# Kernel tuning notes

Measured on AMD Instinct MI355X. Metric: run time of the kernel, lower is better.

The kernel has to match this reference:

```python
import jax, jax.numpy as jnp
import numpy as np

B, T, I, H, O = 8192, 180, 7, 64, 16

def setup_inputs() -> dict:
    key = jax.random.key(0)
    ks = jax.random.split(key, 8)
    s_ih = 1.0 / np.sqrt(H)
    x = jax.random.normal(ks[0], (B, T, I), dtype=jnp.float32)
    # PyTorch nn.LSTM param layout: [4H, in] with gate order i, f, g, o
    W_ih = jax.random.uniform(ks[1], (4 * H, I), jnp.float32, -s_ih, s_ih)
    W_hh = jax.random.uniform(ks[2], (4 * H, H), jnp.float32, -s_ih, s_ih)
    b_ih = jax.random.uniform(ks[3], (4 * H,), jnp.float32, -s_ih, s_ih)
    b_hh = jax.random.uniform(ks[4], (4 * H,), jnp.float32, -s_ih, s_ih)
    W_fc = jax.random.uniform(ks[5], (O, H), jnp.float32, -s_ih, s_ih)
    b_fc = jax.random.uniform(ks[6], (O,), jnp.float32, -s_ih, s_ih)
    return {"x": x, "W_ih": W_ih, "W_hh": W_hh, "b_ih": b_ih,
            "b_hh": b_hh, "W_fc": W_fc, "b_fc": b_fc}

def reference(x, W_ih, W_hh, b_ih, b_hh, W_fc, b_fc):
    x = x.reshape(-1, T, I)
    b = b_ih + b_hh
    # precompute input projections for all timesteps: [T, B, 4H]
    xg = jnp.einsum('bti,gi->tbg', x, W_ih) + b

    def step(carry, xg_t):
        h, c = carry
        gates = xg_t + h @ W_hh.T  # [B, 4H]
        i_g, f_g, g_g, o_g = jnp.split(gates, 4, axis=-1)
        i_g = jax.nn.sigmoid(i_g)
        f_g = jax.nn.sigmoid(f_g)
        g_g = jnp.tanh(g_g)
        o_g = jax.nn.sigmoid(o_g)
        c = f_g * c + i_g * g_g
        h = o_g * jnp.tanh(c)
        return (h, c), None

    h0 = jnp.zeros((x.shape[0], H), dtype=x.dtype)
    c0 = jnp.zeros((x.shape[0], H), dtype=x.dtype)
    (h_last, _), _ = jax.lax.scan(step, (h0, c0), xg)
    return h_last @ W_fc.T + b_fc  # [B, O]
```

## Files before the change

### kernel.cpp

```cpp
#include <hip/hip_runtime.h>
#include <math.h>

#ifndef __has_builtin
#define __has_builtin(x) 0
#endif

#if __has_builtin(__builtin_amdgcn_rcpf)
#define FAST_RCP(x) __builtin_amdgcn_rcpf(x)
#else
#define FAST_RCP(x) (1.0f / (x))
#endif

#if __has_builtin(__builtin_amdgcn_exp2f)
#define FAST_EXP2(x) __builtin_amdgcn_exp2f(x)
#else
#define FAST_EXP2(x) exp2f(x)
#endif

typedef _Float16 half8 __attribute__((ext_vector_type(8)));
typedef _Float16 half2v __attribute__((ext_vector_type(2)));
typedef float f32x4 __attribute__((ext_vector_type(4)));
typedef float f32x2 __attribute__((ext_vector_type(2)));

constexpr int T_STEPS  = 180;
constexpr int I_DIM    = 7;
constexpr int HDIM     = 64;
constexpr int BT       = 16;
constexpr int BSTRIDE  = 104;

__global__ __launch_bounds__(512, 4) void lstm_mfma_kernel(
    const float* __restrict__ x,
    const float* __restrict__ W_ih,
    const float* __restrict__ W_hh,
    const float* __restrict__ b_ih,
    const float* __restrict__ b_hh,
    const float* __restrict__ W_fc,
    const float* __restrict__ b_fc,
    float* __restrict__ out) {
    __shared__ alignas(16) _Float16 Blds[2][BT][BSTRIDE];
    __shared__ alignas(16) float hlds[BT][HDIM + 4];

    const int tid  = (int)threadIdx.x;
    const int w    = tid >> 6;
    const int lane = tid & 63;
    const int q    = lane >> 4;
    const int n15  = lane & 15;
    const long bbase = (long)blockIdx.x * BT;

    half8 afrag[2][3];
#pragma unroll
    for (int pt = 0; pt < 2; ++pt) {
        const int rq   = n15 >> 2;
        const int gate = n15 & 3;
        const int unit = 8 * w + 2 * rq + pt;
        const int grow = gate * HDIM + unit;
        const float scl = (gate == 2) ? 2.88539008177792681472f
                                      : -1.44269504088896340736f;
#pragma unroll
        for (int kc = 0; kc < 3; ++kc) {
#pragma unroll
            for (int j = 0; j < 8; ++j) {
                const int k = kc * 32 + q * 8 + j;
                float v;
                if (k < I_DIM)            v = W_ih[grow * I_DIM + k];
                else if (k == I_DIM)      v = b_ih[grow] + b_hh[grow];
                else if (k < 8 + HDIM)    v = W_hh[grow * HDIM + (k - 8)];
                else                      v = 0.0f;
                afrag[pt][kc][j] = (_Float16)(scl * v);
            }
        }
    }

    for (int idx = tid; idx < 2 * BT * BSTRIDE; idx += 512) {
        const int buf = idx / (BT * BSTRIDE);
        const int rem = idx % (BT * BSTRIDE);
        const int n = rem / BSTRIDE, k = rem % BSTRIDE;
        float v = 0.0f;
        if (k == I_DIM)                 v = 1.0f;
        else if (k < I_DIM && buf == 0) v = x[(bbase + n) * (T_STEPS * I_DIM) + k];
        Blds[buf][n][k] = (_Float16)v;
    }
    __syncthreads();

    const int u0 = 8 * w + 2 * q;

    const _Float16* const rb0 = &Blds[0][n15][q * 8];
    const _Float16* const rb1 = &Blds[1][n15][q * 8];
    half2v* const hw0 = (half2v*)&Blds[0][n15][8 + u0];
    half2v* const hw1 = (half2v*)&Blds[1][n15][8 + u0];

    const int xn = tid >> 3, xi7 = tid & 7;
    const int xi_ld = (xi7 < I_DIM) ? xi7 : I_DIM - 1;
    const int xi_st = (xi7 < I_DIM) ? xi7 : 96 + xn % 8;
    const bool xact = (tid < 128);
    const float* const xcol = x + (bbase + xn) * (T_STEPS * I_DIM) + xi_ld;
    _Float16* const xw0 = &Blds[0][xn][xi_st];
    _Float16* const xw1 = &Blds[1][xn][xi_st];

    float xA = xact ? xcol[1 * I_DIM] : 0.0f;
    float xB = xact ? xcol[2 * I_DIM] : 0.0f;

    float c0 = 0.0f, c1 = 0.0f, h0 = 0.0f, h1 = 0.0f;

#define LSTM_CELL(ACC, CREG, HREG)                                             \
    {                                                                          \
        const float A = FAST_EXP2(ACC[0]);                                     \
        const float F = FAST_EXP2(ACC[1]);                                     \
        const float E = FAST_EXP2(ACC[2]);                                     \
        const float P = (1.0f + A) * (E + 1.0f);                               \
        const float Q = 1.0f + F;                                              \
        const float R = FAST_RCP(P * Q);                                       \
        CREG = (CREG * P + (E - 1.0f) * Q) * R;                                \
        const float O = FAST_EXP2(ACC[3]);                                     \
        float cs = 2.88539008177792681472f * CREG;                             \
        cs = fminf(fmaxf(cs, -80.0f), 80.0f);                                  \
        const float C = FAST_EXP2(cs);                                         \
        HREG = (C - 1.0f) * FAST_RCP((1.0f + O) * (C + 1.0f));                 \
    }

#define LSTM_STEP(TT, RB, HW, XW, XREG)                                        \
    {                                                                          \
        const half8 bf0 = *(const half8*)(RB);                                 \
        const half8 bf1 = *(const half8*)((RB) + 32);                          \
        const half8 bf2 = *(const half8*)((RB) + 64);                          \
        if (xact) {                                                            \
            *(XW) = (_Float16)XREG;                                            \
            int tl = (TT) + 3;                                                 \
            if (tl >= T_STEPS) tl = T_STEPS - 1;                               \
            XREG = xcol[tl * I_DIM];                                           \
        }                                                                      \
        f32x4 acc0 = {0.f, 0.f, 0.f, 0.f};                                     \
        f32x4 acc1 = {0.f, 0.f, 0.f, 0.f};                                     \
        acc0 = __builtin_amdgcn_mfma_f32_16x16x32_f16(afrag[0][0], bf0, acc0, 0, 0, 0); \
        acc1 = __builtin_amdgcn_mfma_f32_16x16x32_f16(afrag[1][0], bf0, acc1, 0, 0, 0); \
        acc0 = __builtin_amdgcn_mfma_f32_16x16x32_f16(afrag[0][1], bf1, acc0, 0, 0, 0); \
        acc1 = __builtin_amdgcn_mfma_f32_16x16x32_f16(afrag[1][1], bf1, acc1, 0, 0, 0); \
        acc0 = __builtin_amdgcn_mfma_f32_16x16x32_f16(afrag[0][2], bf2, acc0, 0, 0, 0); \
        acc1 = __builtin_amdgcn_mfma_f32_16x16x32_f16(afrag[1][2], bf2, acc1, 0, 0, 0); \
        LSTM_CELL(acc0, c0, h0)                                                \
        LSTM_CELL(acc1, c1, h1)                                                \
        *(HW) = (half2v){(_Float16)h0, (_Float16)h1};                          \
        __syncthreads();                                                       \
    }

    for (int t = 0; t < T_STEPS; t += 2) {
        LSTM_STEP(t, rb0, hw1, xw1, xA)
        LSTM_STEP(t + 1, rb1, hw0, xw0, xB)
    }
#undef LSTM_STEP
#undef LSTM_CELL

    *(f32x2*)&hlds[n15][u0] = (f32x2){h0, h1};
    __syncthreads();
    if (tid < 256) {
        const int b = tid >> 4, j = tid & 15;
        float s = b_fc[j];
#pragma unroll 8
        for (int u = 0; u < HDIM; ++u)
            s += hlds[b][u] * W_fc[j * HDIM + u];
        out[(bbase + b) * 16 + j] = s;
    }
}

extern "C" void kernel_launch(void* const* d_in, const int* in_sizes, int n_in,
                              void* d_out, int out_size, void* d_ws, size_t ws_size,
                              hipStream_t stream) {
    const float* x    = (const float*)d_in[0];
    const float* W_ih = (const float*)d_in[1];
    const float* W_hh = (const float*)d_in[2];
    const float* b_ih = (const float*)d_in[3];
    const float* b_hh = (const float*)d_in[4];
    const float* W_fc = (const float*)d_in[5];
    const float* b_fc = (const float*)d_in[6];
    float* out = (float*)d_out;

    const int B = in_sizes[0] / (T_STEPS * I_DIM);
    const int grid = B / BT;

    lstm_mfma_kernel<<<grid, 512, 0, stream>>>(x, W_ih, W_hh, b_ih, b_hh,
                                               W_fc, b_fc, out);
}
```

Baseline: 198.2 us.

## Preload full x sequence into LDS and share reciprocals across cell pairs

Before the recurrence, the kernel copies the block's whole input sequence into LDS as fp16, with a constant-one column for the bias. This replaces the per-step global loads and LDS writes of x that a subset of threads did. The K layout changes so x and bias occupy the first 32-wide MFMA chunk, read from the x buffer or a zero pad, and h takes the remaining two chunks. The two LSTM cells each thread owns are computed together so each reciprocal is shared between them. Clamps are simplified to one-sided mins. In exchange, LDS use grows by about 46KB per block, which may limit occupancy.

```diff
diff --git a/kernel.cpp b/kernel.cpp
--- a/kernel.cpp
+++ b/kernel.cpp
@@ -24,9 +24,10 @@
 
 constexpr int T_STEPS  = 180;
 constexpr int I_DIM    = 7;
+constexpr int XLEN     = T_STEPS * I_DIM;
 constexpr int HDIM     = 64;
 constexpr int BT       = 16;
-constexpr int BSTRIDE  = 104;
+constexpr int HSTRIDE  = 72;
 
 __global__ __launch_bounds__(512, 4) void lstm_mfma_kernel(
     const float* __restrict__ x,
@@ -37,7 +38,9 @@
     const float* __restrict__ W_fc,
     const float* __restrict__ b_fc,
     float* __restrict__ out) {
-    __shared__ alignas(16) _Float16 Blds[2][BT][BSTRIDE];
+    __shared__ alignas(16) _Float16 xlds[T_STEPS][BT][8];
+    __shared__ alignas(16) _Float16 Blds[2][BT][HSTRIDE];
+    __shared__ alignas(16) _Float16 zpad[32];
     __shared__ alignas(16) float hlds[BT][HDIM + 4];
 
     const int tid  = (int)threadIdx.x;
@@ -62,93 +65,87 @@
             for (int j = 0; j < 8; ++j) {
                 const int k = kc * 32 + q * 8 + j;
                 float v;
-                if (k < I_DIM)            v = W_ih[grow * I_DIM + k];
-                else if (k == I_DIM)      v = b_ih[grow] + b_hh[grow];
-                else if (k < 8 + HDIM)    v = W_hh[grow * HDIM + (k - 8)];
-                else                      v = 0.0f;
+                if (k < I_DIM)        v = W_ih[grow * I_DIM + k];
+                else if (k == I_DIM)  v = b_ih[grow] + b_hh[grow];
+                else if (k < 32)      v = 0.0f;
+                else                  v = W_hh[grow * HDIM + (k - 32)];
                 afrag[pt][kc][j] = (_Float16)(scl * v);
             }
         }
     }
 
-    for (int idx = tid; idx < 2 * BT * BSTRIDE; idx += 512) {
-        const int buf = idx / (BT * BSTRIDE);
-        const int rem = idx % (BT * BSTRIDE);
-        const int n = rem / BSTRIDE, k = rem % BSTRIDE;
-        float v = 0.0f;
-        if (k == I_DIM)                 v = 1.0f;
-        else if (k < I_DIM && buf == 0) v = x[(bbase + n) * (T_STEPS * I_DIM) + k];
-        Blds[buf][n][k] = (_Float16)v;
+    for (int idx = tid; idx < BT * XLEN; idx += 512) {
+        const int n = idx / XLEN, r = idx % XLEN;
+        const int t = r / I_DIM, i = r % I_DIM;
+        xlds[t][n][i] = (_Float16)x[(bbase + n) * XLEN + r];
     }
+    for (int idx = tid; idx < T_STEPS * BT; idx += 512)
+        xlds[idx >> 4][idx & 15][7] = (_Float16)1.0f;
+    if (tid < 32) zpad[tid] = (_Float16)0.0f;
+    for (int idx = tid; idx < 2 * BT * HSTRIDE; idx += 512)
+        (&Blds[0][0][0])[idx] = (_Float16)0.0f;
     __syncthreads();
 
     const int u0 = 8 * w + 2 * q;
 
-    const _Float16* const rb0 = &Blds[0][n15][q * 8];
-    const _Float16* const rb1 = &Blds[1][n15][q * 8];
-    half2v* const hw0 = (half2v*)&Blds[0][n15][8 + u0];
-    half2v* const hw1 = (half2v*)&Blds[1][n15][8 + u0];
-
-    const int xn = tid >> 3, xi7 = tid & 7;
-    const int xi_ld = (xi7 < I_DIM) ? xi7 : I_DIM - 1;
-    const int xi_st = (xi7 < I_DIM) ? xi7 : 96 + xn % 8;
-    const bool xact = (tid < 128);
-    const float* const xcol = x + (bbase + xn) * (T_STEPS * I_DIM) + xi_ld;
-    _Float16* const xw0 = &Blds[0][xn][xi_st];
-    _Float16* const xw1 = &Blds[1][xn][xi_st];
-
-    float xA = xact ? xcol[1 * I_DIM] : 0.0f;
-    float xB = xact ? xcol[2 * I_DIM] : 0.0f;
+    const _Float16* xp = (q == 0) ? &xlds[0][n15][0] : &zpad[(q - 1) * 8];
+    const int xstep = (q == 0) ? (BT * 8) : 0;
+    const _Float16* const r0a = &Blds[0][n15][0];
+    const _Float16* const r0b = &Blds[0][n15][32];
+    const _Float16* const r1a = &Blds[1][n15][0];
+    const _Float16* const r1b = &Blds[1][n15][32];
+    half2v* const hw0 = (half2v*)&Blds[0][n15][u0];
+    half2v* const hw1 = (half2v*)&Blds[1][n15][u0];
 
     float c0 = 0.0f, c1 = 0.0f, h0 = 0.0f, h1 = 0.0f;
 
-#define LSTM_CELL(ACC, CREG, HREG)                                             \
+#define LSTM_CELLPAIR(ACC0, ACC1)                                              \
     {                                                                          \
-        const float A = FAST_EXP2(ACC[0]);                                     \
-        const float F = FAST_EXP2(ACC[1]);                                     \
-        const float E = FAST_EXP2(ACC[2]);                                     \
-        const float P = (1.0f + A) * (E + 1.0f);                               \
-        const float Q = 1.0f + F;                                              \
-        const float R = FAST_RCP(P * Q);                                       \
-        CREG = (CREG * P + (E - 1.0f) * Q) * R;                                \
-        const float O = FAST_EXP2(ACC[3]);                                     \
-        float cs = 2.88539008177792681472f * CREG;                             \
-        cs = fminf(fmaxf(cs, -80.0f), 80.0f);                                  \
-        const float C = FAST_EXP2(cs);                                         \
-        HREG = (C - 1.0f) * FAST_RCP((1.0f + O) * (C + 1.0f));                 \
+        const float A0 = FAST_EXP2(ACC0[0]), A1 = FAST_EXP2(ACC1[0]);          \
+        const float F0 = FAST_EXP2(ACC0[1]), F1 = FAST_EXP2(ACC1[1]);          \
+        const float E0 = FAST_EXP2(fminf(ACC0[2], 30.0f));                     \
+        const float E1 = FAST_EXP2(fminf(ACC1[2], 30.0f));                     \
+        const float P0 = (1.0f + A0) * (E0 + 1.0f), Q0 = 1.0f + F0;            \
+        const float P1 = (1.0f + A1) * (E1 + 1.0f), Q1 = 1.0f + F1;            \
+        const float PQ0 = P0 * Q0, PQ1 = P1 * Q1;                              \
+        const float R = FAST_RCP(PQ0 * PQ1);                                   \
+        c0 = (c0 * P0 + (E0 - 1.0f) * Q0) * (R * PQ1);                         \
+        c1 = (c1 * P1 + (E1 - 1.0f) * Q1) * (R * PQ0);                         \
+        const float O0 = FAST_EXP2(ACC0[3]), O1 = FAST_EXP2(ACC1[3]);          \
+        const float C0 = FAST_EXP2(fminf(2.88539008177792681472f * c0, 30.0f));\
+        const float C1 = FAST_EXP2(fminf(2.88539008177792681472f * c1, 30.0f));\
+        const float d0 = (1.0f + O0) * (C0 + 1.0f);                            \
+        const float d1 = (1.0f + O1) * (C1 + 1.0f);                            \
+        const float Rh = FAST_RCP(d0 * d1);                                    \
+        h0 = (C0 - 1.0f) * (Rh * d1);                                          \
+        h1 = (C1 - 1.0f) * (Rh * d0);                                          \
     }
 
-#define LSTM_STEP(TT, RB, HW, XW, XREG)                                        \
+#define LSTM_STEP(RA, RB, HW)                                                  \
     {                                                                          \
-        const half8 bf0 = *(const half8*)(RB);                                 \
-        const half8 bf1 = *(const half8*)((RB) + 32);                          \
-        const half8 bf2 = *(const half8*)((RB) + 64);                          \
-        if (xact) {                                                            \
-            *(XW) = (_Float16)XREG;                                            \
-            int tl = (TT) + 3;                                                 \
-            if (tl >= T_STEPS) tl = T_STEPS - 1;                               \
-            XREG = xcol[tl * I_DIM];                                           \
-        }                                                                      \
+        const half8 bfx = *(const half8*)xp;                                   \
+        xp += xstep;                                                           \
+        const half8 bf1 = *(const half8*)((RA) + q * 8);                       \
+        const half8 bf2 = *(const half8*)((RB) + q * 8);                       \
         f32x4 acc0 = {0.f, 0.f, 0.f, 0.f};                                     \
         f32x4 acc1 = {0.f, 0.f, 0.f, 0.f};                                     \
-        acc0 = __builtin_amdgcn_mfma_f32_16x16x32_f16(afrag[0][0], bf0, acc0, 0, 0, 0); \
-        acc1 = __builtin_amdgcn_mfma_f32_16x16x32_f16(afrag[1][0], bf0, acc1, 0, 0, 0); \
+        acc0 = __builtin_amdgcn_mfma_f32_16x16x32_f16(afrag[0][0], bfx, acc0, 0, 0, 0); \
+        acc1 = __builtin_amdgcn_mfma_f32_16x16x32_f16(afrag[1][0], bfx, acc1, 0, 0, 0); \
         acc0 = __builtin_amdgcn_mfma_f32_16x16x32_f16(afrag[0][1], bf1, acc0, 0, 0, 0); \
         acc1 = __builtin_amdgcn_mfma_f32_16x16x32_f16(afrag[1][1], bf1, acc1, 0, 0, 0); \
         acc0 = __builtin_amdgcn_mfma_f32_16x16x32_f16(afrag[0][2], bf2, acc0, 0, 0, 0); \
         acc1 = __builtin_amdgcn_mfma_f32_16x16x32_f16(afrag[1][2], bf2, acc1, 0, 0, 0); \
-        LSTM_CELL(acc0, c0, h0)                                                \
-        LSTM_CELL(acc1, c1, h1)                                                \
+        LSTM_CELLPAIR(acc0, acc1)                                              \
         *(HW) = (half2v){(_Float16)h0, (_Float16)h1};                          \
         __syncthreads();                                                       \
     }
 
     for (int t = 0; t < T_STEPS; t += 2) {
-        LSTM_STEP(t, rb0, hw1, xw1, xA)
-        LSTM_STEP(t + 1, rb1, hw0, xw0, xB)
+        LSTM_STEP(r0a, r0b, hw1)
+        LSTM_STEP(r1a, r1b, hw0)
     }
 #undef LSTM_STEP
-#undef LSTM_CELL
+#undef LSTM_CELLPAIR
 
     *(f32x2*)&hlds[n15][u0] = (f32x2){h0, h1};
     __syncthreads();
@@ -174,7 +171,7 @@
     const float* b_fc = (const float*)d_in[6];
     float* out = (float*)d_out;
 
-    const int B = in_sizes[0] / (T_STEPS * I_DIM);
+    const int B = in_sizes[0] / XLEN;
     const int grid = B / BT;
 
     lstm_mfma_kernel<<<grid, 512, 0, stream>>>(x, W_ih, W_hh, b_ih, b_hh,
```

New measurement: 199.5 us. About the same (+0.6%).
